# Optimization experiments

Measured on AMD Instinct MI355X. Metric: run time of the kernel, lower is better.

Reference implementation:

```python
import jax, jax.numpy as jnp
import numpy as np

B = 64          # batch
D_FEAT = 512    # resnet18 feature dim before final fc
EMB = 16        # emb_dimension (hardcoded in module)
K = 512         # vqvae_dict_size
P_TOTAL = 1482625  # sum of prod(shape) over all hypernet-generated params


def setup_inputs() -> dict:
    key = jax.random.key(0)
    k1, k2, k3, k4, k5 = jax.random.split(key, 5)
    feat = jax.random.normal(k1, (B, D_FEAT), dtype=jnp.float32)
    fc_w = jax.random.normal(k2, (EMB, D_FEAT), dtype=jnp.float32) * 0.05
    fc_b = jax.random.normal(k3, (EMB,), dtype=jnp.float32) * 0.05
    # nn.init.normal_(embedding.weight, mean=0, std=0.4)
    codebook = jax.random.normal(k4, (K, EMB), dtype=jnp.float32) * 0.4
    # concatenation of all per-parameter generator matrices [EMB, prod(shape_i)]
    Wgen = jax.random.normal(k5, (EMB, P_TOTAL), dtype=jnp.float32) * 0.1
    return {"feat": feat, "fc_w": fc_w, "fc_b": fc_b,
            "codebook": codebook, "Wgen": Wgen}


def reference(feat, fc_w, fc_b, codebook, Wgen):
    # encoder final fc: [B, 512] -> [B, 16]
    embed = feat @ fc_w.T + fc_b  # [B, EMB]

    # VQ: squared L2 distances to codebook, argmin, gather
    d = (jnp.sum(embed * embed, axis=1, keepdims=True)
         + jnp.sum(codebook * codebook, axis=1)
         - 2.0 * embed @ codebook.T)                 # [B, K]
    idx = jnp.argmin(d, axis=1)                      # [B]
    quantized = jnp.take(codebook, idx, axis=0)      # [B, EMB] (== one-hot @ codebook)

    # commitment / codebook losses (F.mse_loss = mean)
    e_latent_loss = jnp.mean((jax.lax.stop_gradient(quantized) - embed) ** 2)
    q_latent_loss = jnp.mean((quantized - jax.lax.stop_gradient(embed)) ** 2)
    loss = q_latent_loss + 0.25 * e_latent_loss

    # straight-through estimator
    quantized_st = embed + jax.lax.stop_gradient(quantized - embed)  # [B, EMB]

    # hypernetwork: all per-parameter matmuls fused into one [B,16]@[16,P_TOTAL]
    gen_weights = quantized_st @ Wgen                # [B, P_TOTAL]
    return gen_weights, loss
```

## Files before the change

### kernel.cpp

```cpp
#include <hip/hip_runtime.h>

#define P_TOT 1482625
#define BATCH 64
#define EMB 16
#define DFEAT 512
#define KCODE 512

__global__ __launch_bounds__(256) void k_embed_vq(
    const float* __restrict__ feat,
    const float* __restrict__ fcw,
    const float* __restrict__ fcb,
    const float* __restrict__ cb,
    float* __restrict__ qws,
    float* __restrict__ loss_part)
{
    const int b   = blockIdx.x;
    const int tid = threadIdx.x;

    __shared__ float red[EMB][17];
    __shared__ float embed_s[EMB];
    __shared__ float dist_s[256];
    __shared__ int   idx_s[256];

    {
        const int e = tid >> 4;
        const int c = tid & 15;
        const float4* fp = (const float4*)(feat + b * DFEAT + c * 32);
        const float4* wp = (const float4*)(fcw  + e * DFEAT + c * 32);
        float acc = 0.f;
#pragma unroll
        for (int j = 0; j < 8; j++) {
            float4 f = fp[j], w = wp[j];
            acc += f.x * w.x + f.y * w.y + f.z * w.z + f.w * w.w;
        }
        red[e][c] = acc;
    }
    __syncthreads();
    if (tid < EMB) {
        float s = fcb[tid];
#pragma unroll
        for (int c = 0; c < 16; c++) s += red[tid][c];
        embed_s[tid] = s;
    }
    __syncthreads();

    float emb[EMB];
#pragma unroll
    for (int e = 0; e < EMB; e++) emb[e] = embed_s[e];

    float bestd = 1e30f;
    int   bestk = 0;
#pragma unroll
    for (int r = 0; r < 2; r++) {
        const int k = tid + r * 256;
        const float4* cp = (const float4*)(cb + k * EMB);
        float d = 0.f;
#pragma unroll
        for (int q = 0; q < 4; q++) {
            float4 cv = cp[q];
            d += cv.x * cv.x - 2.f * cv.x * emb[q * 4 + 0];
            d += cv.y * cv.y - 2.f * cv.y * emb[q * 4 + 1];
            d += cv.z * cv.z - 2.f * cv.z * emb[q * 4 + 2];
            d += cv.w * cv.w - 2.f * cv.w * emb[q * 4 + 3];
        }
        if (d < bestd) { bestd = d; bestk = k; }
    }
    dist_s[tid] = bestd;
    idx_s[tid]  = bestk;
    __syncthreads();

    for (int s = 128; s > 0; s >>= 1) {
        if (tid < s) {
            float od = dist_s[tid + s];
            int   ok = idx_s[tid + s];
            if (od < dist_s[tid] || (od == dist_s[tid] && ok < idx_s[tid])) {
                dist_s[tid] = od;
                idx_s[tid]  = ok;
            }
        }
        __syncthreads();
    }

    if (tid == 0) {
        const int kb = idx_s[0];
        float l = 0.f;
#pragma unroll
        for (int e = 0; e < EMB; e++) {
            float qv = cb[kb * EMB + e];
            qws[b * EMB + e] = qv;
            float dd = qv - embed_s[e];
            l += dd * dd;
        }
        loss_part[b] = l;
    }
}

__global__ __launch_bounds__(256) void k_gen(
    const float* __restrict__ Wgen,
    const float* __restrict__ qws,
    const float* __restrict__ loss_part,
    float* __restrict__ out)
{
    if (blockIdx.x == 0) {
        if (threadIdx.x < 64) {
            float v = loss_part[threadIdx.x];
#pragma unroll
            for (int o = 32; o > 0; o >>= 1) v += __shfl_down(v, o, 64);
            if (threadIdx.x == 0)
                out[(size_t)BATCH * P_TOT] = 1.25f * v * (1.0f / 1024.0f);
        }
        return;
    }

    const int lane = threadIdx.x & 63;
    const int wv   = threadIdx.x >> 6;
    const int myc  = wv * 256 + lane;
    const size_t col0 = (size_t)(blockIdx.x - 1) * 1024;

    if (col0 + 1024 <= (size_t)P_TOT) {
        const float* wp = Wgen + col0 + myc;
        float w[EMB][4];
#pragma unroll
        for (int e = 0; e < EMB; e++) {
            const float* we = wp + (size_t)e * P_TOT;
#pragma unroll
            for (int j = 0; j < 4; j++) w[e][j] = we[j * 64];
        }

        float qn[EMB];
#pragma unroll
        for (int e = 0; e < EMB; e++) qn[e] = qws[e];

        float* op = out + col0 + myc;
#pragma unroll 2
        for (int b = 0; b < BATCH; b++) {
            float qc[EMB];
#pragma unroll
            for (int e = 0; e < EMB; e++) qc[e] = qn[e];

            if (b + 1 < BATCH) {
                const float* q1 = qws + (b + 1) * EMB;
#pragma unroll
                for (int e = 0; e < EMB; e++) qn[e] = q1[e];
            }

            float acc[4] = {0.f, 0.f, 0.f, 0.f};
#pragma unroll
            for (int e = 0; e < EMB; e++) {
                const float qe = qc[e];
#pragma unroll
                for (int j = 0; j < 4; j++) acc[j] = fmaf(qe, w[e][j], acc[j]);
            }
            float* ob = op + (size_t)b * P_TOT;
#pragma unroll
            for (int j = 0; j < 4; j++) ob[j * 64] = acc[j];
        }
    } else {
#pragma unroll
        for (int j = 0; j < 4; j++) {
            const size_t c = col0 + myc + (size_t)j * 64;
            if (c < (size_t)P_TOT) {
                float w1[EMB];
#pragma unroll
                for (int e = 0; e < EMB; e++)
                    w1[e] = Wgen[(size_t)e * P_TOT + c];
                for (int b = 0; b < BATCH; b++) {
                    const float* q = qws + b * EMB;
                    float a = 0.f;
#pragma unroll
                    for (int e = 0; e < EMB; e++) a = fmaf(q[e], w1[e], a);
                    out[(size_t)b * P_TOT + c] = a;
                }
            }
        }
    }
}

extern "C" void kernel_launch(void* const* d_in, const int* in_sizes, int n_in,
                              void* d_out, int out_size, void* d_ws, size_t ws_size,
                              hipStream_t stream) {
    const float* feat = (const float*)d_in[0];
    const float* fcw  = (const float*)d_in[1];
    const float* fcb  = (const float*)d_in[2];
    const float* cb   = (const float*)d_in[3];
    const float* wgen = (const float*)d_in[4];
    float* out = (float*)d_out;

    float* qws   = (float*)d_ws;
    float* lpart = qws + BATCH * EMB;

    k_embed_vq<<<BATCH, 256, 0, stream>>>(feat, fcw, fcb, cb, qws, lpart);

    const int colblocks = (P_TOT + 1023) / 1024;
    k_gen<<<colblocks + 1, 256, 0, stream>>>(wgen, qws, lpart, out);
}
```

Measured before the change: 474.2 us.

## Split generator into batch-residue classes for aligned float4 output stores

Since P_TOT is odd, rows of the output are misaligned for vector stores. The change splits batch rows by b mod 4 so each class starts at a column offset that makes out row addresses 16-byte aligned, enabling float4 stores, and loads Wgen with misalignment-compensating paired f4 loads. Leftover edge columns are handled by a special block. This trades one launch for four launches and reads Wgen four times, with extra load work for unaligned rows.

```diff
diff --git a/kernel.cpp b/kernel.cpp
--- a/kernel.cpp
+++ b/kernel.cpp
@@ -5,6 +5,8 @@
 #define EMB 16
 #define DFEAT 512
 #define KCODE 512
+
+typedef float f4 __attribute__((ext_vector_type(4)));
 
 __global__ __launch_bounds__(256) void k_embed_vq(
     const float* __restrict__ feat,
@@ -95,84 +97,99 @@
     }
 }
 
-__global__ __launch_bounds__(256) void k_gen(
+__device__ const int g_pcls[12] = {0, 1,1,1,1,1, 2,2,2,2,2, 3};
+__device__ const int g_pcol[12] = {1482624,
+                                   0, 1, 2, 1482623, 1482624,
+                                   0, 1, 1482622, 1482623, 1482624,
+                                   0};
+
+template<int R>
+__global__ __launch_bounds__(256) void k_gen_cls(
     const float* __restrict__ Wgen,
     const float* __restrict__ qws,
     const float* __restrict__ loss_part,
     float* __restrict__ out)
 {
-    if (blockIdx.x == 0) {
-        if (threadIdx.x < 64) {
-            float v = loss_part[threadIdx.x];
-#pragma unroll
-            for (int o = 32; o > 0; o >>= 1) v += __shfl_down(v, o, 64);
-            if (threadIdx.x == 0)
-                out[(size_t)BATCH * P_TOT] = 1.25f * v * (1.0f / 1024.0f);
-        }
-        return;
-    }
-
-    const int lane = threadIdx.x & 63;
-    const int wv   = threadIdx.x >> 6;
-    const int myc  = wv * 256 + lane;
-    const size_t col0 = (size_t)(blockIdx.x - 1) * 1024;
-
-    if (col0 + 1024 <= (size_t)P_TOT) {
-        const float* wp = Wgen + col0 + myc;
-        float w[EMB][4];
+    constexpr int SR = (4 - R) & 3;
+    constexpr long long NR = ((long long)P_TOT - SR) / 4;
+
+    int bid = blockIdx.x;
+    if (R == 0) {
+        if (bid == 0) {
+            const int tid = threadIdx.x;
+            if (tid < 64) {
+                float v = loss_part[tid];
+#pragma unroll
+                for (int o = 32; o > 0; o >>= 1) v += __shfl_down(v, o, 64);
+                if (tid == 0)
+                    out[(size_t)BATCH * P_TOT] = 1.25f * v * (1.0f / 1024.0f);
+            } else if (tid < 64 + 192) {
+                const int idx = tid - 64;
+                const int p = idx >> 4, u = idx & 15;
+                const int b = g_pcls[p] + 4 * u;
+                const size_t col = (size_t)g_pcol[p];
+                float a = 0.f;
+#pragma unroll
+                for (int e = 0; e < EMB; e++)
+                    a = fmaf(qws[b * EMB + e], Wgen[(size_t)e * P_TOT + col], a);
+                out[(size_t)b * P_TOT + col] = a;
+            }
+            return;
+        }
+        bid -= 1;
+    }
+
+    const long long slot = (long long)bid * 256 + threadIdx.x;
+    if (slot >= NR) return;
+    const size_t S = (size_t)SR + 4 * (size_t)slot;
+
+    float w[EMB][4];
+    if (slot != NR - 1) {
 #pragma unroll
         for (int e = 0; e < EMB; e++) {
-            const float* we = wp + (size_t)e * P_TOT;
-#pragma unroll
-            for (int j = 0; j < 4; j++) w[e][j] = we[j * 64];
-        }
-
-        float qn[EMB];
-#pragma unroll
-        for (int e = 0; e < EMB; e++) qn[e] = qws[e];
-
-        float* op = out + col0 + myc;
+            const int m = (e + SR) & 3;
+            const float* rowp = Wgen + (size_t)e * P_TOT + (S - (size_t)m);
+            f4 lo = *(const f4*)rowp;
+            f4 hi = {0.f, 0.f, 0.f, 0.f};
+            if (m) hi = *(const f4*)(rowp + 4);
+#pragma unroll
+            for (int c = 0; c < 4; c++)
+                w[e][c] = (m + c < 4) ? lo[m + c] : hi[m + c - 4];
+        }
+    } else {
+#pragma unroll
+        for (int e = 0; e < EMB; e++)
+#pragma unroll
+            for (int c = 0; c < 4; c++)
+                w[e][c] = Wgen[(size_t)e * P_TOT + S + c];
+    }
+
+    float qn[EMB];
+#pragma unroll
+    for (int e = 0; e < EMB; e++) qn[e] = qws[R * EMB + e];
+
 #pragma unroll 2
-        for (int b = 0; b < BATCH; b++) {
-            float qc[EMB];
-#pragma unroll
-            for (int e = 0; e < EMB; e++) qc[e] = qn[e];
-
-            if (b + 1 < BATCH) {
-                const float* q1 = qws + (b + 1) * EMB;
-#pragma unroll
-                for (int e = 0; e < EMB; e++) qn[e] = q1[e];
-            }
-
-            float acc[4] = {0.f, 0.f, 0.f, 0.f};
-#pragma unroll
-            for (int e = 0; e < EMB; e++) {
-                const float qe = qc[e];
-#pragma unroll
-                for (int j = 0; j < 4; j++) acc[j] = fmaf(qe, w[e][j], acc[j]);
-            }
-            float* ob = op + (size_t)b * P_TOT;
-#pragma unroll
-            for (int j = 0; j < 4; j++) ob[j * 64] = acc[j];
-        }
-    } else {
-#pragma unroll
-        for (int j = 0; j < 4; j++) {
-            const size_t c = col0 + myc + (size_t)j * 64;
-            if (c < (size_t)P_TOT) {
-                float w1[EMB];
-#pragma unroll
-                for (int e = 0; e < EMB; e++)
-                    w1[e] = Wgen[(size_t)e * P_TOT + c];
-                for (int b = 0; b < BATCH; b++) {
-                    const float* q = qws + b * EMB;
-                    float a = 0.f;
-#pragma unroll
-                    for (int e = 0; e < EMB; e++) a = fmaf(q[e], w1[e], a);
-                    out[(size_t)b * P_TOT + c] = a;
-                }
-            }
-        }
+    for (int u = 0; u < 16; u++) {
+        const int b = R + 4 * u;
+        float qc[EMB];
+#pragma unroll
+        for (int e = 0; e < EMB; e++) qc[e] = qn[e];
+        if (u + 1 < 16) {
+            const float* q1 = qws + (b + 4) * EMB;
+#pragma unroll
+            for (int e = 0; e < EMB; e++) qn[e] = q1[e];
+        }
+
+        f4 acc = {0.f, 0.f, 0.f, 0.f};
+#pragma unroll
+        for (int e = 0; e < EMB; e++) {
+            const float qe = qc[e];
+            acc[0] = fmaf(qe, w[e][0], acc[0]);
+            acc[1] = fmaf(qe, w[e][1], acc[1]);
+            acc[2] = fmaf(qe, w[e][2], acc[2]);
+            acc[3] = fmaf(qe, w[e][3], acc[3]);
+        }
+        *(f4*)(out + (size_t)b * P_TOT + S) = acc;
     }
 }
 
@@ -191,6 +208,8 @@
 
     k_embed_vq<<<BATCH, 256, 0, stream>>>(feat, fcw, fcb, cb, qws, lpart);
 
-    const int colblocks = (P_TOT + 1023) / 1024;
-    k_gen<<<colblocks + 1, 256, 0, stream>>>(wgen, qws, lpart, out);
+    k_gen_cls<0><<<1449, 256, 0, stream>>>(wgen, qws, lpart, out);
+    k_gen_cls<1><<<1448, 256, 0, stream>>>(wgen, qws, lpart, out);
+    k_gen_cls<2><<<1448, 256, 0, stream>>>(wgen, qws, lpart, out);
+    k_gen_cls<3><<<1448, 256, 0, stream>>>(wgen, qws, lpart, out);
 }
```

Measured after the change: 511.4 us. +7.9%, slower.
